# Performance work log

Measured on AMD Instinct MI355X. Metric: run time of the kernel, lower is better.

Reference implementation:

```python
import jax, jax.numpy as jnp
import numpy as np

N_NODES = 100000
N_EDGES = 1600000
N_FEAT = 64
HID = 64
HL = 256
N_GRAPHS = 512


def _lin(k, i, o):
    return (jax.random.normal(k, (i, o), jnp.float32) / np.sqrt(i)).astype(jnp.float32)


def setup_inputs() -> dict:
    key = jax.random.key(0)
    ks = jax.random.split(key, 20)
    inp = {
        "x": jax.random.normal(ks[0], (N_NODES, N_FEAT), jnp.float32),
        "edge_index": jax.random.randint(ks[1], (2, N_EDGES), 0, N_NODES),
        "batch": jnp.sort(jax.random.randint(ks[2], (N_NODES,), 0, N_GRAPHS)),
        "T": jax.random.normal(ks[3], (N_GRAPHS, 1), jnp.float32),
    }
    dims = [(N_FEAT, HID), (HID, HID), (HID, HID), (HID, HID)]
    for i, (di, do) in enumerate(dims):
        inp[f"wrel{i}"] = _lin(ks[4 + 3 * i], di, do)
        inp[f"brel{i}"] = jnp.zeros((do,), jnp.float32)
        inp[f"wroot{i}"] = _lin(ks[5 + 3 * i], di, do)
    inp["w1"] = _lin(ks[16], 3 * HID + 1, HL)
    inp["b1"] = jnp.zeros((HL,), jnp.float32)
    inp["w2"] = _lin(ks[17], HL, HL)
    inp["b2"] = jnp.zeros((HL,), jnp.float32)
    inp["w3"] = _lin(ks[18], HL, 1)
    inp["b3"] = jnp.zeros((1,), jnp.float32)
    return inp


def reference(x, edge_index, batch, T,
              wrel0, brel0, wroot0,
              wrel1, brel1, wroot1,
              wrel2, brel2, wroot2,
              wrel3, brel3, wroot3,
              w1, b1, w2, b2, w3, b3):
    src, dst = edge_index[0], edge_index[1]

    def conv(h, wr, br, wq):
        # PyG GraphConv: W_root h_i + W_rel * sum_{j->i} h_j + b_rel
        agg = jax.ops.segment_sum(h[src], dst, num_segments=N_NODES)
        return agg @ wr + br + h @ wq

    h = jax.nn.relu(conv(x, wrel0, brel0, wroot0))
    h = jax.nn.relu(conv(h, wrel1, brel1, wroot1))
    h = jax.nn.relu(conv(h, wrel2, brel2, wroot2))
    h = conv(h, wrel3, brel3, wroot3)  # no relu on conv2 (matches original)

    # global add / mean / max pools over graph ids
    s = jax.ops.segment_sum(h, batch, num_segments=N_GRAPHS)
    cnt = jax.ops.segment_sum(jnp.ones((N_NODES, 1), h.dtype), batch, num_segments=N_GRAPHS)
    mean = s / jnp.maximum(cnt, 1.0)
    mx = jax.ops.segment_max(h, batch, num_segments=N_GRAPHS)
    mx = jnp.where(jnp.isfinite(mx), mx, 0.0)  # empty segments -> 0

    out = jnp.concatenate([mx, mean, s, T], axis=1)  # [G, 3*HID+1]
    o = jax.nn.relu(out @ w1 + b1)
    o = jax.nn.relu(o @ w2 + b2)  # dropout is identity in eval mode
    return o @ w3 + b3
```

## Files before the change

### kernel.cpp

```cpp
#include <hip/hip_runtime.h>
#include <hip/hip_bf16.h>
#include <math.h>

#define N_NODES 100000
#define N_EDGES 1600000
#define N_FEAT 64
#define HID 64
#define HL 256
#define N_GRAPHS 512

#define BUCKET_BITS 7
#define BUCKET_SIZE 128
#define NB ((N_NODES + BUCKET_SIZE - 1) / BUCKET_SIZE)
#define LOFS_W (NB + 1)
#define CAP 3584
#define LREC_CAP 3584
#define EDGES_PER_BLOCK 4096
#define SCAT_BLOCKS ((N_EDGES + EDGES_PER_BLOCK - 1) / EDGES_PER_BLOCK)
#define F2B_BLOCKS (N_NODES * 16 / 256)
#define WPREP_BLOCKS 128
#define ZOFF ((unsigned int)N_NODES * 128u)

typedef short vbf8 __attribute__((ext_vector_type(8)));
typedef float vf4 __attribute__((ext_vector_type(4)));
typedef float vf2 __attribute__((ext_vector_type(2)));

__device__ __forceinline__ unsigned short f2b(float f) {
    unsigned int u = __float_as_uint(f);
    return (unsigned short)((u + 0x7FFFu + ((u >> 16) & 1u)) >> 16);
}
__device__ __forceinline__ float b2f(unsigned short u) {
    return __uint_as_float(((unsigned int)u) << 16);
}
__device__ __forceinline__ unsigned pk2(float lo, float hi) {
    float2 f; f.x = lo; f.y = hi;
    __hip_bfloat162 h = __float22bfloat162_rn(f);
    unsigned r;
    __builtin_memcpy(&r, &h, 4);
    return r;
}
__device__ __forceinline__ vf2 bpair(unsigned int d) {
    vf2 r;
    r.x = __uint_as_float(d << 16);
    r.y = __uint_as_float(d & 0xFFFF0000u);
    return r;
}


__global__ __launch_bounds__(256) void k_mega(
        const int* __restrict__ src, const int* __restrict__ dst,
        int* __restrict__ lofs, unsigned int* __restrict__ ebuf,
        const float4* __restrict__ x, uint2* __restrict__ xb,
        const float* __restrict__ wroot0, const float* __restrict__ wrel0,
        const float* __restrict__ wroot1, const float* __restrict__ wrel1,
        const float* __restrict__ wroot2, const float* __restrict__ wrel2,
        const float* __restrict__ wroot3, const float* __restrict__ wrel3,
        unsigned short* __restrict__ wt) {
    __shared__ int lh[NB];
    __shared__ int lsc[256];
    __shared__ unsigned lrec[EDGES_PER_BLOCK];
    int bid = blockIdx.x;
    int t = threadIdx.x;

    if (bid < SCAT_BLOCKS) {
        for (int i = t; i < NB; i += 256) lh[i] = 0;
        __syncthreads();
        int i0 = bid * EDGES_PER_BLOCK;
        int i1 = min(N_EDGES, i0 + EDGES_PER_BLOCK);
        int cnt = i1 - i0;
        for (int i = i0 + t; i < i1; i += 256)
            atomicAdd(&lh[dst[i] >> BUCKET_BITS], 1);
        __syncthreads();
        int v[4];
        int s = 0;
        int base4 = t * 4;
#pragma unroll
        for (int j = 0; j < 4; j++) {
            v[j] = (base4 + j < NB) ? lh[base4 + j] : 0;
            s += v[j];
        }
        lsc[t] = s;
        __syncthreads();
        for (int off = 1; off < 256; off <<= 1) {
            int xx = lsc[t];
            int y = (t >= off) ? lsc[t - off] : 0;
            __syncthreads();
            lsc[t] = xx + y;
            __syncthreads();
        }
        int run = lsc[t] - s;
        int* lrow = lofs + (size_t)bid * LOFS_W;
#pragma unroll
        for (int j = 0; j < 4; j++) {
            int b = base4 + j;
            if (b < NB) {
                lrow[b] = run;
                lh[b] = run;
            }
            run += v[j];
        }
        if (t == 255) lrow[NB] = cnt;
        __syncthreads();
        for (int i = i0 + t; i < i1; i += 256) {
            int sN = src[i], d = dst[i];
            int b = d >> BUCKET_BITS;
            int p = atomicAdd(&lh[b], 1);
            lrec[p] = ((unsigned)sN << 7) | (unsigned)(d & 127);
        }
        __syncthreads();
        unsigned* eb = ebuf + (size_t)bid * EDGES_PER_BLOCK;
        for (int j = t; j < cnt; j += 256) eb[j] = lrec[j];
    } else if (bid < SCAT_BLOCKS + F2B_BLOCKS) {
        int i = (bid - SCAT_BLOCKS) * 256 + t;
        if (i < N_NODES * 16) {
            float4 v = x[i];
            uint2 o;
            o.x = pk2(v.x, v.y);
            o.y = pk2(v.z, v.w);
            xb[i] = o;
        }
    } else {
        int gi = (bid - SCAT_BLOCKS - F2B_BLOCKS) * 256 + t;
        if (gi < 4 * 64 * 128) {
            int layer = gi >> 13;
            int i = gi & 8191;
            int nn = i >> 7, k = i & 127;
            const float* wr = (layer == 0) ? wroot0 : (layer == 1) ? wroot1
                             : (layer == 2) ? wroot2 : wroot3;
            const float* wl = (layer == 0) ? wrel0 : (layer == 1) ? wrel1
                             : (layer == 2) ? wrel2 : wrel3;
            float v = (k < 64) ? wr[k * 64 + nn] : wl[(k - 64) * 64 + nn];
            wt[gi] = f2b(v);
        }
    }
}


__global__ __launch_bounds__(256) void k_fscatter2(
        const unsigned int* __restrict__ ebuf, const int* __restrict__ lofs,
        int2* __restrict__ re, unsigned int* __restrict__ soff,
        unsigned short* __restrict__ hbA, unsigned short* __restrict__ hbB, int n) {
    __shared__ int rcnt[512];
    __shared__ int rbase[512];
    __shared__ int rpre[512];
    __shared__ int tsc[256];
    __shared__ unsigned lrec[LREC_CAP];
    __shared__ int lcnt[BUCKET_SIZE];
    __shared__ int sc[BUCKET_SIZE];
    __shared__ int cur[BUCKET_SIZE];
    int b = blockIdx.x;
    int n0 = b * BUCKET_SIZE;
    int t = threadIdx.x;
    if (b == 0 && t < 16) {
        uint4 z = make_uint4(0u, 0u, 0u, 0u);
        unsigned short* hp = (t < 8) ? hbA : hbB;
        ((uint4*)(hp + (size_t)N_NODES * 64))[t & 7] = z;
    }
    for (int blk = t; blk < 512; blk += 256) {
        int c = 0, ba = 0;
        if (blk < SCAT_BLOCKS) {
            const int* lr = lofs + (size_t)blk * LOFS_W + b;
            ba = lr[0];
            c = lr[1] - ba;
        }
        rcnt[blk] = c;
        rbase[blk] = ba;
    }
    __syncthreads();
    int c0 = rcnt[2 * t], c1 = rcnt[2 * t + 1];
    tsc[t] = c0 + c1;
    __syncthreads();
    for (int off = 1; off < 256; off <<= 1) {
        int xx = tsc[t];
        int y = (t >= off) ? tsc[t - off] : 0;
        __syncthreads();
        tsc[t] = xx + y;
        __syncthreads();
    }
    int ex = tsc[t] - (c0 + c1);
    rpre[2 * t] = ex;
    rpre[2 * t + 1] = ex + c0;
    __syncthreads();
    int cb = tsc[255];
    for (int blk = t; blk < SCAT_BLOCKS; blk += 256) {
        int c = rcnt[blk];
        int dsto = rpre[blk];
        const unsigned* sp = ebuf + (size_t)blk * EDGES_PER_BLOCK + rbase[blk];
        for (int j = 0; j < c; j++) lrec[dsto + j] = sp[j];
    }
    if (t < BUCKET_SIZE) lcnt[t] = 0;
    __syncthreads();
    for (int r = t; r < cb; r += 256)
        atomicAdd(&lcnt[lrec[r] & 127u], 1);
    __syncthreads();
    int v = 0, pcnt = 0;
    if (t < BUCKET_SIZE) {
        v = lcnt[t];
        pcnt = (v + 7) & ~7;
        sc[t] = pcnt;
    }
    __syncthreads();
    for (int off = 1; off < BUCKET_SIZE; off <<= 1) {
        int xx = 0;
        if (t < BUCKET_SIZE) {
            xx = sc[t];
            if (t >= off) xx += sc[t - off];
        }
        __syncthreads();
        if (t < BUCKET_SIZE) sc[t] = xx;
        __syncthreads();
    }
    if (t < BUCKET_SIZE) {
        int start = b * CAP + sc[t] - pcnt;
        if (n0 + t < n) re[n0 + t] = make_int2(start, start + v);
        cur[t] = start;
        for (int z = start + v; z < start + pcnt; z++) soff[z] = ZOFF;
    }
    __syncthreads();
    for (int r = t; r < cb; r += 256) {
        unsigned rec = lrec[r];
        int p = atomicAdd(&cur[rec & 127u], 1);
        soff[p] = rec & ~127u;
    }
}


__global__ __launch_bounds__(256) void k_agg(
    const unsigned short* __restrict__ hb, unsigned short* __restrict__ aggb,
    const int2* __restrict__ re, const unsigned int* __restrict__ soff, int n) {
    int lane = threadIdx.x & 63;
    int i = (blockIdx.x * 256 + threadIdx.x) >> 6;
    if (i >= n) return;
    int q = lane >> 3;
    int sl = lane & 7;
    int2 bounds = re[i];
    int e0 = bounds.x, e1 = bounds.y;
    int iters = (e1 - e0 + 7) >> 3;
    const char* base = (const char*)hb + sl * 16;

    vf2 A[4], B[4];
#pragma unroll
    for (int f = 0; f < 4; f++) { A[f] = (vf2){0.f, 0.f}; B[f] = (vf2){0.f, 0.f}; }

    int eq = e0 + q;
    int it = 0;
    for (; it + 2 <= iters; it += 2) {
        int ea = eq + it * 8, eb = ea + 8;
        unsigned oa = __builtin_nontemporal_load(soff + ea);
        unsigned ob = __builtin_nontemporal_load(soff + eb);
        uint4 da = *(const uint4*)(base + oa);
        uint4 db = *(const uint4*)(base + ob);
        A[0] += bpair(da.x); A[1] += bpair(da.y);
        A[2] += bpair(da.z); A[3] += bpair(da.w);
        B[0] += bpair(db.x); B[1] += bpair(db.y);
        B[2] += bpair(db.z); B[3] += bpair(db.w);
    }
    if (it < iters) {
        int ea = eq + it * 8;
        unsigned oa = __builtin_nontemporal_load(soff + ea);
        uint4 da = *(const uint4*)(base + oa);
        A[0] += bpair(da.x); A[1] += bpair(da.y);
        A[2] += bpair(da.z); A[3] += bpair(da.w);
    }

    float f[8];
#pragma unroll
    for (int k = 0; k < 4; k++) {
        vf2 s2 = A[k] + B[k];
        float slo = s2.x, shi = s2.y;
        slo += __shfl_xor(slo, 8);
        slo += __shfl_xor(slo, 16);
        slo += __shfl_xor(slo, 32);
        shi += __shfl_xor(shi, 8);
        shi += __shfl_xor(shi, 16);
        shi += __shfl_xor(shi, 32);
        f[2 * k] = slo;
        f[2 * k + 1] = shi;
    }
    if (q == 0) {
        uint4 o;
        o.x = pk2(f[0], f[1]);
        o.y = pk2(f[2], f[3]);
        o.z = pk2(f[4], f[5]);
        o.w = pk2(f[6], f[7]);
        *(uint4*)((char*)aggb + (size_t)i * 128 + sl * 16) = o;
    }
}


template <int RELU>
__global__ __launch_bounds__(256) void k_gemm(
    const unsigned short* __restrict__ hb, const unsigned short* __restrict__ aggb,
    const unsigned short* __restrict__ wt, const float* __restrict__ brel,
    unsigned short* __restrict__ hbout, int n) {
    __shared__ float sc[4][16 * 68];

    int tid = threadIdx.x;
    int w = tid >> 6, l = tid & 63;
    int lm = l & 15, q = l >> 4;
    int r0 = blockIdx.x * 64 + w * 16;

    int arow = r0 + lm;
    if (arow >= n) arow = n - 1;
    const unsigned short* ah = hb + (size_t)arow * 64 + q * 8;
    const unsigned short* aa = aggb + (size_t)arow * 64 + q * 8;
    vbf8 afr[4];
    afr[0] = *(const vbf8*)(ah);
    afr[1] = *(const vbf8*)(ah + 32);
    afr[2] = *(const vbf8*)(aa);
    afr[3] = *(const vbf8*)(aa + 32);

    vf4 acc[4];
#pragma unroll
    for (int t = 0; t < 4; t++) acc[t] = (vf4){0.f, 0.f, 0.f, 0.f};

#pragma unroll
    for (int t = 0; t < 4; t++) {
        const unsigned short* wrow = wt + (size_t)(t * 16 + lm) * 128 + q * 8;
#pragma unroll
        for (int s = 0; s < 4; s++) {
            vbf8 bfr = *(const vbf8*)(wrow + s * 32);
            acc[t] = __builtin_amdgcn_mfma_f32_16x16x32_bf16(afr[s], bfr, acc[t], 0, 0, 0);
        }
    }

    float* sw_ = sc[w];
#pragma unroll
    for (int t = 0; t < 4; t++) {
        float b = brel[t * 16 + lm];
#pragma unroll
        for (int i = 0; i < 4; i++) {
            float v = acc[t][i] + b;
            if (RELU) v = fmaxf(v, 0.f);
            sw_[(q * 4 + i) * 68 + t * 16 + lm] = v;
        }
    }
    int rr = l >> 2, cs = l & 3;
    int node = r0 + rr;
    if (node < n) {
        const float* rp = sw_ + rr * 68 + cs * 16;
        float4 v0 = *(const float4*)(rp);
        float4 v1 = *(const float4*)(rp + 4);
        float4 v2 = *(const float4*)(rp + 8);
        float4 v3 = *(const float4*)(rp + 12);
        uint4 o0, o1;
        o0.x = pk2(v0.x, v0.y);
        o0.y = pk2(v0.z, v0.w);
        o0.z = pk2(v1.x, v1.y);
        o0.w = pk2(v1.z, v1.w);
        o1.x = pk2(v2.x, v2.y);
        o1.y = pk2(v2.z, v2.w);
        o1.z = pk2(v3.x, v3.y);
        o1.w = pk2(v3.z, v3.w);
        uint4* op = (uint4*)(hbout + (size_t)node * 64 + cs * 16);
        op[0] = o0;
        op[1] = o1;
    }
}


__global__ __launch_bounds__(256) void k_poolmlp(
    const unsigned short* __restrict__ hb, const int* __restrict__ batch,
    const float* __restrict__ T, const float* __restrict__ w1,
    const float* __restrict__ b1, const float* __restrict__ w2,
    const float* __restrict__ b2, const float* __restrict__ w3,
    const float* __restrict__ b3, float* __restrict__ out, int n) {
    __shared__ float psum[4][64];
    __shared__ float pmax[4][64];
    __shared__ float sin_[200];
    __shared__ float so1[256];
    __shared__ float red[256];
    int g = blockIdx.x, t = threadIdx.x;
    int l = t & 63, c = t >> 6;

    int lo = 0, hi = n;
    while (lo < hi) { int m = (lo + hi) >> 1; if (batch[m] < g) lo = m + 1; else hi = m; }
    int s0 = lo;
    int lo2 = s0, hi2 = n;
    while (lo2 < hi2) { int m = (lo2 + hi2) >> 1; if (batch[m] < g + 1) lo2 = m + 1; else hi2 = m; }
    int s1 = lo2;

    float sa0 = 0.f, sa1 = 0.f, sa2 = 0.f, sa3 = 0.f;
    float ma0 = -INFINITY, ma1 = -INFINITY, ma2 = -INFINITY, ma3 = -INFINITY;
    int nn = s0 + c;
    for (; nn + 12 < s1; nn += 16) {
        float v0 = b2f(hb[(size_t)nn * 64 + l]);
        float v1 = b2f(hb[(size_t)(nn + 4) * 64 + l]);
        float v2 = b2f(hb[(size_t)(nn + 8) * 64 + l]);
        float v3 = b2f(hb[(size_t)(nn + 12) * 64 + l]);
        sa0 += v0; sa1 += v1; sa2 += v2; sa3 += v3;
        ma0 = fmaxf(ma0, v0); ma1 = fmaxf(ma1, v1);
        ma2 = fmaxf(ma2, v2); ma3 = fmaxf(ma3, v3);
    }
    for (; nn < s1; nn += 4) {
        float v = b2f(hb[(size_t)nn * 64 + l]);
        sa0 += v;
        ma0 = fmaxf(ma0, v);
    }
    psum[c][l] = (sa0 + sa1) + (sa2 + sa3);
    pmax[c][l] = fmaxf(fmaxf(ma0, ma1), fmaxf(ma2, ma3));
    __syncthreads();
    if (t < 64) {
        float s = (psum[0][t] + psum[1][t]) + (psum[2][t] + psum[3][t]);
        float mx = fmaxf(fmaxf(pmax[0][t], pmax[1][t]), fmaxf(pmax[2][t], pmax[3][t]));
        int cnt = s1 - s0;
        float mean = s / fmaxf((float)cnt, 1.f);
        if (cnt == 0) mx = 0.f;
        sin_[t] = mx;
        sin_[64 + t] = mean;
        sin_[128 + t] = s;
        if (t == 0) {
            sin_[192] = T[g];
#pragma unroll
            for (int z = 193; z < 200; z++) sin_[z] = 0.f;
        }
    }
    __syncthreads();

    float a = b1[t];
    {
        float wv[8];
        for (int k = 0; k < 192; k += 8) {
#pragma unroll
            for (int u = 0; u < 8; u++) wv[u] = w1[(k + u) * 256 + t];
#pragma unroll
            for (int u = 0; u < 8; u++) a += sin_[k + u] * wv[u];
        }
        a += sin_[192] * w1[192 * 256 + t];
    }
    a = fmaxf(a, 0.f);
    so1[t] = a;
    __syncthreads();

    float a2 = b2[t];
    {
        float wv[8];
        for (int k = 0; k < 256; k += 8) {
#pragma unroll
            for (int u = 0; u < 8; u++) wv[u] = w2[(k + u) * 256 + t];
#pragma unroll
            for (int u = 0; u < 8; u++) a2 += so1[k + u] * wv[u];
        }
    }
    a2 = fmaxf(a2, 0.f);
    red[t] = a2 * w3[t];
    __syncthreads();
    for (int s = 128; s > 0; s >>= 1) {
        if (t < s) red[t] += red[t + s];
        __syncthreads();
    }
    if (t == 0) out[g] = red[0] + b3[0];
}

extern "C" void kernel_launch(void* const* d_in, const int* in_sizes, int n_in,
                              void* d_out, int out_size, void* d_ws, size_t ws_size,
                              hipStream_t stream) {
    const int N = N_NODES, E = N_EDGES, G = N_GRAPHS;

    const float* x = (const float*)d_in[0];
    const int* ei = (const int*)d_in[1];
    const int* batch = (const int*)d_in[2];
    const float* T = (const float*)d_in[3];
    const float* wrel[4] = {(const float*)d_in[4], (const float*)d_in[7],
                            (const float*)d_in[10], (const float*)d_in[13]};
    const float* brel[4] = {(const float*)d_in[5], (const float*)d_in[8],
                            (const float*)d_in[11], (const float*)d_in[14]};
    const float* wroot[4] = {(const float*)d_in[6], (const float*)d_in[9],
                             (const float*)d_in[12], (const float*)d_in[15]};
    const float* w1 = (const float*)d_in[16];
    const float* b1 = (const float*)d_in[17];
    const float* w2 = (const float*)d_in[18];
    const float* b2 = (const float*)d_in[19];
    const float* w3 = (const float*)d_in[20];
    const float* b3 = (const float*)d_in[21];
    float* out = (float*)d_out;

    const int* esrc = ei;
    const int* edst = ei + E;

    char* ws = (char*)d_ws;
    size_t off = 0;
    auto alloc = [&](size_t bytes) {
        size_t r = off;
        off = (off + bytes + 255) & ~(size_t)255;
        return r;
    };
    int* lofs = (int*)(ws + alloc((size_t)SCAT_BLOCKS * LOFS_W * 4));
    int2* re = (int2*)(ws + alloc((size_t)N * 8));
    unsigned int* soff = (unsigned int*)(ws + alloc((size_t)NB * CAP * 4));
    unsigned int* ebuf = (unsigned int*)(ws + alloc((size_t)SCAT_BLOCKS * EDGES_PER_BLOCK * 4));
    unsigned short* hbA = (unsigned short*)(ws + alloc((size_t)N * 64 * 2 + 128));
    unsigned short* hbB = (unsigned short*)(ws + alloc((size_t)N * 64 * 2 + 128));
    unsigned short* aggb = (unsigned short*)(ws + alloc((size_t)N * 64 * 2));
    unsigned short* wt = (unsigned short*)(ws + alloc((size_t)4 * 64 * 128 * 2));

    k_mega<<<SCAT_BLOCKS + F2B_BLOCKS + WPREP_BLOCKS, 256, 0, stream>>>(
        esrc, edst, lofs, ebuf, (const float4*)x, (uint2*)hbA,
        wroot[0], wrel[0], wroot[1], wrel[1],
        wroot[2], wrel[2], wroot[3], wrel[3], wt);
    k_fscatter2<<<NB, 256, 0, stream>>>(ebuf, lofs, re, soff, hbA, hbB, N);

    int agg_blocks = (N * 64 + 255) / 256;
    int gemm_blocks = (N + 63) / 64;

    k_agg<<<agg_blocks, 256, 0, stream>>>(hbA, aggb, re, soff, N);
    k_gemm<1><<<gemm_blocks, 256, 0, stream>>>(hbA, aggb, wt + 0 * 8192, brel[0], hbB, N);

    k_agg<<<agg_blocks, 256, 0, stream>>>(hbB, aggb, re, soff, N);
    k_gemm<1><<<gemm_blocks, 256, 0, stream>>>(hbB, aggb, wt + 1 * 8192, brel[1], hbA, N);

    k_agg<<<agg_blocks, 256, 0, stream>>>(hbA, aggb, re, soff, N);
    k_gemm<1><<<gemm_blocks, 256, 0, stream>>>(hbA, aggb, wt + 2 * 8192, brel[2], hbB, N);

    k_agg<<<agg_blocks, 256, 0, stream>>>(hbB, aggb, re, soff, N);
    k_gemm<0><<<gemm_blocks, 256, 0, stream>>>(hbB, aggb, wt + 3 * 8192, brel[3], hbA, N);

    k_poolmlp<<<G, 256, 0, stream>>>(hbA, batch, T, w1, b1, w2, b2, w3, b3, out, N);
}
```

Measured before the change: 399.7 us.

## Split node features into four 16-feature planes for cache-friendly gather aggregation

Stores the bf16 node features and aggregates in four separate feature planes of 16 features (32 bytes per node). The aggregation kernel now gives each block one plane and has each wave process four nodes at once, with 16 edge lanes of 8 bytes each. Edge lists are padded to multiples of 16, and the edge offsets are rescaled to the 32-byte row stride. Each plane's working set (about 3.2 MB) is smaller, so random gathers should hit cache more often. The cost is reading the edge list four times, narrower 8-byte loads, and load imbalance within a wave when the four nodes have different degrees.

```diff
diff --git a/kernel.cpp b/kernel.cpp
--- a/kernel.cpp
+++ b/kernel.cpp
@@ -13,13 +13,18 @@
 #define BUCKET_SIZE 128
 #define NB ((N_NODES + BUCKET_SIZE - 1) / BUCKET_SIZE)
 #define LOFS_W (NB + 1)
-#define CAP 3584
+#define CAP 4608
 #define LREC_CAP 3584
 #define EDGES_PER_BLOCK 4096
 #define SCAT_BLOCKS ((N_EDGES + EDGES_PER_BLOCK - 1) / EDGES_PER_BLOCK)
 #define F2B_BLOCKS (N_NODES * 16 / 256)
 #define WPREP_BLOCKS 128
-#define ZOFF ((unsigned int)N_NODES * 128u)
+
+#define PSTR 3200256u
+#define PSTRU (PSTR / 2)
+#define ASTR 3200000u
+#define ASTRU (ASTR / 2)
+#define ZOFF32 ((unsigned)N_NODES * 32u)
 
 typedef short vbf8 __attribute__((ext_vector_type(8)));
 typedef float vf4 __attribute__((ext_vector_type(4)));
@@ -50,7 +55,7 @@
 __global__ __launch_bounds__(256) void k_mega(
         const int* __restrict__ src, const int* __restrict__ dst,
         int* __restrict__ lofs, unsigned int* __restrict__ ebuf,
-        const float4* __restrict__ x, uint2* __restrict__ xb,
+        const float4* __restrict__ x, unsigned short* __restrict__ xb,
         const float* __restrict__ wroot0, const float* __restrict__ wrel0,
         const float* __restrict__ wroot1, const float* __restrict__ wrel1,
         const float* __restrict__ wroot2, const float* __restrict__ wrel2,
@@ -114,10 +119,12 @@
         int i = (bid - SCAT_BLOCKS) * 256 + t;
         if (i < N_NODES * 16) {
             float4 v = x[i];
+            int node = i >> 4, kc = i & 15;
             uint2 o;
             o.x = pk2(v.x, v.y);
             o.y = pk2(v.z, v.w);
-            xb[i] = o;
+            *(uint2*)((char*)xb + (size_t)(kc >> 2) * PSTR +
+                      (size_t)node * 32 + (kc & 3) * 8) = o;
         }
     } else {
         int gi = (bid - SCAT_BLOCKS - F2B_BLOCKS) * 256 + t;
@@ -151,10 +158,13 @@
     int b = blockIdx.x;
     int n0 = b * BUCKET_SIZE;
     int t = threadIdx.x;
-    if (b == 0 && t < 16) {
+    if (b == 0 && t < 8) {
+        int plane = t & 3;
+        unsigned short* hp = (t < 4) ? hbA : hbB;
         uint4 z = make_uint4(0u, 0u, 0u, 0u);
-        unsigned short* hp = (t < 8) ? hbA : hbB;
-        ((uint4*)(hp + (size_t)N_NODES * 64))[t & 7] = z;
+        uint4* zp = (uint4*)((char*)hp + (size_t)plane * PSTR + (size_t)N_NODES * 32);
+        zp[0] = z;
+        zp[1] = z;
     }
     for (int blk = t; blk < 512; blk += 256) {
         int c = 0, ba = 0;
@@ -196,7 +206,7 @@
     int v = 0, pcnt = 0;
     if (t < BUCKET_SIZE) {
         v = lcnt[t];
-        pcnt = (v + 7) & ~7;
+        pcnt = (v + 15) & ~15;
         sc[t] = pcnt;
     }
     __syncthreads();
@@ -214,13 +224,13 @@
         int start = b * CAP + sc[t] - pcnt;
         if (n0 + t < n) re[n0 + t] = make_int2(start, start + v);
         cur[t] = start;
-        for (int z = start + v; z < start + pcnt; z++) soff[z] = ZOFF;
+        for (int z = start + v; z < start + pcnt; z++) soff[z] = ZOFF32;
     }
     __syncthreads();
     for (int r = t; r < cb; r += 256) {
         unsigned rec = lrec[r];
         int p = atomicAdd(&cur[rec & 127u], 1);
-        soff[p] = rec & ~127u;
+        soff[p] = (rec >> 7) * 32u;
     }
 }
 
@@ -228,62 +238,77 @@
 __global__ __launch_bounds__(256) void k_agg(
     const unsigned short* __restrict__ hb, unsigned short* __restrict__ aggb,
     const int2* __restrict__ re, const unsigned int* __restrict__ soff, int n) {
-    int lane = threadIdx.x & 63;
-    int i = (blockIdx.x * 256 + threadIdx.x) >> 6;
-    if (i >= n) return;
-    int q = lane >> 3;
-    int sl = lane & 7;
-    int2 bounds = re[i];
-    int e0 = bounds.x, e1 = bounds.y;
-    int iters = (e1 - e0 + 7) >> 3;
-    const char* base = (const char*)hb + sl * 16;
-
-    vf2 A[4], B[4];
-#pragma unroll
-    for (int f = 0; f < 4; f++) { A[f] = (vf2){0.f, 0.f}; B[f] = (vf2){0.f, 0.f}; }
-
-    int eq = e0 + q;
-    int it = 0;
-    for (; it + 2 <= iters; it += 2) {
-        int ea = eq + it * 8, eb = ea + 8;
-        unsigned oa = __builtin_nontemporal_load(soff + ea);
-        unsigned ob = __builtin_nontemporal_load(soff + eb);
-        uint4 da = *(const uint4*)(base + oa);
-        uint4 db = *(const uint4*)(base + ob);
-        A[0] += bpair(da.x); A[1] += bpair(da.y);
-        A[2] += bpair(da.z); A[3] += bpair(da.w);
-        B[0] += bpair(db.x); B[1] += bpair(db.y);
-        B[2] += bpair(db.z); B[3] += bpair(db.w);
-    }
-    if (it < iters) {
-        int ea = eq + it * 8;
-        unsigned oa = __builtin_nontemporal_load(soff + ea);
-        uint4 da = *(const uint4*)(base + oa);
-        A[0] += bpair(da.x); A[1] += bpair(da.y);
-        A[2] += bpair(da.z); A[3] += bpair(da.w);
-    }
-
-    float f[8];
-#pragma unroll
-    for (int k = 0; k < 4; k++) {
-        vf2 s2 = A[k] + B[k];
-        float slo = s2.x, shi = s2.y;
-        slo += __shfl_xor(slo, 8);
-        slo += __shfl_xor(slo, 16);
-        slo += __shfl_xor(slo, 32);
-        shi += __shfl_xor(shi, 8);
-        shi += __shfl_xor(shi, 16);
-        shi += __shfl_xor(shi, 32);
-        f[2 * k] = slo;
-        f[2 * k + 1] = shi;
+    int l = threadIdx.x & 63;
+    int w = threadIdx.x >> 6;
+    int s = blockIdx.x & 3;
+    int i0 = (blockIdx.x >> 2) * 16 + w * 4;
+    if (i0 >= n) return;
+    int q = l >> 2, sl = l & 3;
+    const char* base = (const char*)hb + (size_t)s * PSTR + sl * 8;
+
+    int2 b0 = re[i0];
+    int2 b1 = re[min(i0 + 1, n - 1)];
+    int2 b2 = re[min(i0 + 2, n - 1)];
+    int2 b3 = re[min(i0 + 3, n - 1)];
+    int it0 = (b0.y - b0.x + 15) >> 4;
+    int it1 = (i0 + 1 < n) ? (b1.y - b1.x + 15) >> 4 : 0;
+    int it2 = (i0 + 2 < n) ? (b2.y - b2.x + 15) >> 4 : 0;
+    int it3 = (i0 + 3 < n) ? (b3.y - b3.x + 15) >> 4 : 0;
+    int iters = max(max(it0, it1), max(it2, it3));
+
+    vf2 acc[4][2];
+#pragma unroll
+    for (int j = 0; j < 4; j++) {
+        acc[j][0] = (vf2){0.f, 0.f};
+        acc[j][1] = (vf2){0.f, 0.f};
+    }
+
+    for (int it = 0; it < iters; it++) {
+        int step = it * 16 + q;
+        unsigned o0 = soff[(it < it0) ? (b0.x + step) : 0];
+        unsigned o1 = soff[(it < it1) ? (b1.x + step) : 0];
+        unsigned o2 = soff[(it < it2) ? (b2.x + step) : 0];
+        unsigned o3 = soff[(it < it3) ? (b3.x + step) : 0];
+        if (it >= it0) o0 = ZOFF32;
+        if (it >= it1) o1 = ZOFF32;
+        if (it >= it2) o2 = ZOFF32;
+        if (it >= it3) o3 = ZOFF32;
+        uint2 d0 = *(const uint2*)(base + o0);
+        uint2 d1 = *(const uint2*)(base + o1);
+        uint2 d2 = *(const uint2*)(base + o2);
+        uint2 d3 = *(const uint2*)(base + o3);
+        acc[0][0] += bpair(d0.x); acc[0][1] += bpair(d0.y);
+        acc[1][0] += bpair(d1.x); acc[1][1] += bpair(d1.y);
+        acc[2][0] += bpair(d2.x); acc[2][1] += bpair(d2.y);
+        acc[3][0] += bpair(d3.x); acc[3][1] += bpair(d3.y);
+    }
+
+    float f[4][4];
+#pragma unroll
+    for (int j = 0; j < 4; j++) {
+        float a0 = acc[j][0].x, a1 = acc[j][0].y;
+        float a2 = acc[j][1].x, a3 = acc[j][1].y;
+        a0 += __shfl_xor(a0, 4);  a0 += __shfl_xor(a0, 8);
+        a0 += __shfl_xor(a0, 16); a0 += __shfl_xor(a0, 32);
+        a1 += __shfl_xor(a1, 4);  a1 += __shfl_xor(a1, 8);
+        a1 += __shfl_xor(a1, 16); a1 += __shfl_xor(a1, 32);
+        a2 += __shfl_xor(a2, 4);  a2 += __shfl_xor(a2, 8);
+        a2 += __shfl_xor(a2, 16); a2 += __shfl_xor(a2, 32);
+        a3 += __shfl_xor(a3, 4);  a3 += __shfl_xor(a3, 8);
+        a3 += __shfl_xor(a3, 16); a3 += __shfl_xor(a3, 32);
+        f[j][0] = a0; f[j][1] = a1; f[j][2] = a2; f[j][3] = a3;
     }
     if (q == 0) {
-        uint4 o;
-        o.x = pk2(f[0], f[1]);
-        o.y = pk2(f[2], f[3]);
-        o.z = pk2(f[4], f[5]);
-        o.w = pk2(f[6], f[7]);
-        *(uint4*)((char*)aggb + (size_t)i * 128 + sl * 16) = o;
+        char* ab = (char*)aggb + (size_t)s * ASTR + sl * 8;
+#pragma unroll
+        for (int j = 0; j < 4; j++) {
+            if (i0 + j < n) {
+                uint2 o;
+                o.x = pk2(f[j][0], f[j][1]);
+                o.y = pk2(f[j][2], f[j][3]);
+                *(uint2*)(ab + (size_t)(i0 + j) * 32) = o;
+            }
+        }
     }
 }
 
@@ -302,13 +327,14 @@
 
     int arow = r0 + lm;
     if (arow >= n) arow = n - 1;
-    const unsigned short* ah = hb + (size_t)arow * 64 + q * 8;
-    const unsigned short* aa = aggb + (size_t)arow * 64 + q * 8;
+    size_t rowoff = (size_t)arow * 16;
+    int p0 = q >> 1;
+    int half = (q & 1) * 8;
     vbf8 afr[4];
-    afr[0] = *(const vbf8*)(ah);
-    afr[1] = *(const vbf8*)(ah + 32);
-    afr[2] = *(const vbf8*)(aa);
-    afr[3] = *(const vbf8*)(aa + 32);
+    afr[0] = *(const vbf8*)(hb + (size_t)p0 * PSTRU + rowoff + half);
+    afr[1] = *(const vbf8*)(hb + (size_t)(p0 + 2) * PSTRU + rowoff + half);
+    afr[2] = *(const vbf8*)(aggb + (size_t)p0 * ASTRU + rowoff + half);
+    afr[3] = *(const vbf8*)(aggb + (size_t)(p0 + 2) * ASTRU + rowoff + half);
 
     vf4 acc[4];
 #pragma unroll
@@ -352,9 +378,9 @@
         o1.y = pk2(v2.z, v2.w);
         o1.z = pk2(v3.x, v3.y);
         o1.w = pk2(v3.z, v3.w);
-        uint4* op = (uint4*)(hbout + (size_t)node * 64 + cs * 16);
-        op[0] = o0;
-        op[1] = o1;
+        char* outb = (char*)hbout + (size_t)cs * PSTR + (size_t)node * 32;
+        *(uint4*)outb = o0;
+        *(uint4*)(outb + 16) = o1;
     }
 }
 
@@ -380,20 +406,21 @@
     while (lo2 < hi2) { int m = (lo2 + hi2) >> 1; if (batch[m] < g + 1) lo2 = m + 1; else hi2 = m; }
     int s1 = lo2;
 
+    size_t fb = (size_t)(l >> 4) * PSTRU + (size_t)(l & 15);
     float sa0 = 0.f, sa1 = 0.f, sa2 = 0.f, sa3 = 0.f;
     float ma0 = -INFINITY, ma1 = -INFINITY, ma2 = -INFINITY, ma3 = -INFINITY;
     int nn = s0 + c;
     for (; nn + 12 < s1; nn += 16) {
-        float v0 = b2f(hb[(size_t)nn * 64 + l]);
-        float v1 = b2f(hb[(size_t)(nn + 4) * 64 + l]);
-        float v2 = b2f(hb[(size_t)(nn + 8) * 64 + l]);
-        float v3 = b2f(hb[(size_t)(nn + 12) * 64 + l]);
+        float v0 = b2f(hb[fb + (size_t)nn * 16]);
+        float v1 = b2f(hb[fb + (size_t)(nn + 4) * 16]);
+        float v2 = b2f(hb[fb + (size_t)(nn + 8) * 16]);
+        float v3 = b2f(hb[fb + (size_t)(nn + 12) * 16]);
         sa0 += v0; sa1 += v1; sa2 += v2; sa3 += v3;
         ma0 = fmaxf(ma0, v0); ma1 = fmaxf(ma1, v1);
         ma2 = fmaxf(ma2, v2); ma3 = fmaxf(ma3, v3);
     }
     for (; nn < s1; nn += 4) {
-        float v = b2f(hb[(size_t)nn * 64 + l]);
+        float v = b2f(hb[fb + (size_t)nn * 16]);
         sa0 += v;
         ma0 = fmaxf(ma0, v);
     }
@@ -487,20 +514,20 @@
     };
     int* lofs = (int*)(ws + alloc((size_t)SCAT_BLOCKS * LOFS_W * 4));
     int2* re = (int2*)(ws + alloc((size_t)N * 8));
-    unsigned int* soff = (unsigned int*)(ws + alloc((size_t)NB * CAP * 4));
+    unsigned int* soff = (unsigned int*)(ws + alloc((size_t)NB * CAP * 4 + 8192));
     unsigned int* ebuf = (unsigned int*)(ws + alloc((size_t)SCAT_BLOCKS * EDGES_PER_BLOCK * 4));
-    unsigned short* hbA = (unsigned short*)(ws + alloc((size_t)N * 64 * 2 + 128));
-    unsigned short* hbB = (unsigned short*)(ws + alloc((size_t)N * 64 * 2 + 128));
-    unsigned short* aggb = (unsigned short*)(ws + alloc((size_t)N * 64 * 2));
+    unsigned short* hbA = (unsigned short*)(ws + alloc((size_t)4 * PSTR));
+    unsigned short* hbB = (unsigned short*)(ws + alloc((size_t)4 * PSTR));
+    unsigned short* aggb = (unsigned short*)(ws + alloc((size_t)4 * ASTR));
     unsigned short* wt = (unsigned short*)(ws + alloc((size_t)4 * 64 * 128 * 2));
 
     k_mega<<<SCAT_BLOCKS + F2B_BLOCKS + WPREP_BLOCKS, 256, 0, stream>>>(
-        esrc, edst, lofs, ebuf, (const float4*)x, (uint2*)hbA,
+        esrc, edst, lofs, ebuf, (const float4*)x, hbA,
         wroot[0], wrel[0], wroot[1], wrel[1],
         wroot[2], wrel[2], wroot[3], wrel[3], wt);
     k_fscatter2<<<NB, 256, 0, stream>>>(ebuf, lofs, re, soff, hbA, hbB, N);
 
-    int agg_blocks = (N * 64 + 255) / 256;
+    int agg_blocks = ((N + 15) / 16) * 4;
     int gemm_blocks = (N + 63) / 64;
 
     k_agg<<<agg_blocks, 256, 0, stream>>>(hbA, aggb, re, soff, N);
```

Measured after the change: 522.0 us. +30.6%, slower.
